# Kernel tuning notes

Measured on AMD Instinct MI355X. Metric: run time of the kernel, lower is better.

## Reference

```python
import jax, jax.numpy as jnp
import numpy as np

N = 100000      # nodes
E = 1600000     # edges (avg degree 16)
IN_DIM = 128
HID = 128
OUT = 10
EPS = 1e-5      # BatchNorm eps


def _lin(key, fan_in, fan_out):
    return jax.random.normal(key, (fan_in, fan_out), jnp.float32) * (1.0 / np.sqrt(fan_in))


def setup_inputs() -> dict:
    key = jax.random.key(0)
    ks = jax.random.split(key, 8)
    x = jax.random.normal(ks[0], (N, IN_DIM), jnp.float32)
    edge_index = jax.random.randint(ks[1], (2, E), 0, N, dtype=jnp.int64)
    return {
        "x": x,
        "edge_index": edge_index,
        "W0": _lin(ks[2], IN_DIM, HID), "b0": jnp.zeros((HID,), jnp.float32),
        "g0": jnp.ones((HID,), jnp.float32), "be0": jnp.zeros((HID,), jnp.float32),
        "W1": _lin(ks[3], HID, HID), "b1": jnp.zeros((HID,), jnp.float32),
        "g1": jnp.ones((HID,), jnp.float32), "be1": jnp.zeros((HID,), jnp.float32),
        "W2": _lin(ks[4], HID, OUT), "b2": jnp.zeros((OUT,), jnp.float32),
    }


def gcn_conv(x, W, b, src, dst, n):
    # PyG GCNConv: add self-loops, symmetric normalization D^-1/2 A D^-1/2.
    # deg includes the self-loop (+1).
    e = src.shape[0]
    deg = jax.ops.segment_sum(jnp.ones((e,), x.dtype), dst, num_segments=n) + 1.0
    dinv = jax.lax.rsqrt(deg)                     # deg >= 1 always
    norm = dinv[src] * dinv[dst]                  # [E]
    h = x @ W                                     # [N, out]
    msgs = h[src] * norm[:, None]                 # gather + scale, [E, out]
    agg = jax.ops.segment_sum(msgs, dst, num_segments=n)
    agg = agg + h * (dinv * dinv)[:, None]        # self-loop contribution
    return agg + b


def batch_norm(x, gamma, beta):
    mu = jnp.mean(x, axis=0)
    var = jnp.mean(jnp.square(x - mu), axis=0)    # biased var, as torch BN training
    return gamma * (x - mu) * jax.lax.rsqrt(var + EPS) + beta


def reference(x, edge_index, W0, b0, g0, be0, W1, b1, g1, be1, W2, b2):
    src, dst = edge_index[0], edge_index[1]
    h = jax.nn.relu(batch_norm(gcn_conv(x, W0, b0, src, dst, N), g0, be0))
    h = jax.nn.relu(batch_norm(gcn_conv(h, W1, b1, src, dst, N), g1, be1))
    return gcn_conv(h, W2, b2, src, dst, N)
```

## Files before the change

kernel.cpp:

```cpp
#include <hip/hip_runtime.h>
#include <hip/hip_bf16.h>

static constexpr int NN  = 100000;
static constexpr int NE  = 1600000;
static constexpr int DIM = 128;
static constexpr int OC  = 10;
static constexpr int BK  = 64;
static constexpr float BN_EPS = 1e-5f;
static constexpr float INVN   = 1.0f / (float)NN;

static constexpr int BINS = 391;
static constexpr int CAP  = 8176;
static constexpr int EPB  = 2048;
static constexpr int P1B  = (NE + EPB - 1) / EPB;

typedef unsigned short ushortT;
typedef unsigned int uintT;
typedef __attribute__((ext_vector_type(8))) short short8;
typedef __attribute__((ext_vector_type(4))) float floatx4;

__device__ __forceinline__ ushortT f2bf(float f) {
    union { float f; unsigned int i; } c;
    c.f = f;
    unsigned int r = c.i + 0x7FFFu + ((c.i >> 16) & 1u);
    return (ushortT)(r >> 16);
}

__device__ __forceinline__ uintT pack2(float lo, float hi) {
    return (uintT)f2bf(lo) | ((uintT)f2bf(hi) << 16);
}

__device__ __forceinline__ float4 f4fma(const float4 w, const float s, const float4 acc) {
    float4 r;
    r.x = fmaf(w.x, s, acc.x);
    r.y = fmaf(w.y, s, acc.y);
    r.z = fmaf(w.z, s, acc.z);
    r.w = fmaf(w.w, s, acc.w);
    return r;
}

__device__ __forceinline__ void acc8(const uint4 u, float* a) {
    a[0] += __uint_as_float(u.x << 16);
    a[1] += __uint_as_float(u.x & 0xFFFF0000u);
    a[2] += __uint_as_float(u.y << 16);
    a[3] += __uint_as_float(u.y & 0xFFFF0000u);
    a[4] += __uint_as_float(u.z << 16);
    a[5] += __uint_as_float(u.z & 0xFFFF0000u);
    a[6] += __uint_as_float(u.w << 16);
    a[7] += __uint_as_float(u.w & 0xFFFF0000u);
}

__device__ __forceinline__ void fma8(const uint4 u, float s, float* a) {
    a[0] = fmaf(__uint_as_float(u.x << 16),          s, a[0]);
    a[1] = fmaf(__uint_as_float(u.x & 0xFFFF0000u),  s, a[1]);
    a[2] = fmaf(__uint_as_float(u.y << 16),          s, a[2]);
    a[3] = fmaf(__uint_as_float(u.y & 0xFFFF0000u),  s, a[3]);
    a[4] = fmaf(__uint_as_float(u.z << 16),          s, a[4]);
    a[5] = fmaf(__uint_as_float(u.z & 0xFFFF0000u),  s, a[5]);
    a[6] = fmaf(__uint_as_float(u.w << 16),          s, a[6]);
    a[7] = fmaf(__uint_as_float(u.w & 0xFFFF0000u),  s, a[7]);
}

__device__ __forceinline__ void unp8(const uint4 u, float* a) {
    a[0] = __uint_as_float(u.x << 16);
    a[1] = __uint_as_float(u.x & 0xFFFF0000u);
    a[2] = __uint_as_float(u.y << 16);
    a[3] = __uint_as_float(u.y & 0xFFFF0000u);
    a[4] = __uint_as_float(u.z << 16);
    a[5] = __uint_as_float(u.z & 0xFFFF0000u);
    a[6] = __uint_as_float(u.w << 16);
    a[7] = __uint_as_float(u.w & 0xFFFF0000u);
}

__global__ void k_wt(const float* __restrict__ W0, const float* __restrict__ W1,
                     ushortT* __restrict__ WT0, ushortT* __restrict__ WT1,
                     float* __restrict__ stats) {
    int i = blockIdx.x * 256 + threadIdx.x;
    if (i < 1024) stats[i] = 0.f;
    int half = i >> 14, r = i & 16383;
    int n = r >> 7, k = r & 127;
    if (half == 0) WT0[r] = f2bf(W0[k * 128 + n]);
    else           WT1[r] = f2bf(W1[k * 128 + n]);
}

struct P1S {
    uint2 stage[EPB];
    int lcnt[BINS];
    int lbase[512];
    int lcur[BINS];
    int goff[BINS];
};
union SMu {
    P1S p1;
    ushortT xs[32 * 136];
};

__global__ __launch_bounds__(256)
void k_p1(const int* __restrict__ src, const int* __restrict__ dst,
          uint2* __restrict__ gbin, int* __restrict__ gcur,
          const float* __restrict__ x, const ushortT* __restrict__ WT,
          ushortT* __restrict__ outb)
{
    __shared__ SMu sm;
    const int idx = blockIdx.x;
    const int tid = threadIdx.x;
    const int d5 = idx / 5;
    if (idx - 5 * d5 == 0) {
        P1S& S = sm.p1;
        const int e00 = d5 * EPB;
        for (int b = tid; b < BINS; b += 256) S.lcnt[b] = 0;
        __syncthreads();
        int4 dv[2], sv[2];
        bool val[2];
        #pragma unroll
        for (int i = 0; i < 2; ++i) {
            int e0 = e00 + i * 1024 + tid * 4;
            val[i] = (e0 < NE);
            if (val[i]) {
                dv[i] = *(const int4*)(dst + e0);
                sv[i] = *(const int4*)(src + e0);
                atomicAdd(&S.lcnt[dv[i].x >> 8], 1);
                atomicAdd(&S.lcnt[dv[i].y >> 8], 1);
                atomicAdd(&S.lcnt[dv[i].z >> 8], 1);
                atomicAdd(&S.lcnt[dv[i].w >> 8], 1);
            }
        }
        __syncthreads();
        for (int b = tid; b < 512; b += 256) S.lbase[b] = (b < BINS) ? S.lcnt[b] : 0;
        __syncthreads();
        for (int off = 1; off < 512; off <<= 1) {
            int v0 = (tid >= off) ? S.lbase[tid - off] : 0;
            int c0 = S.lbase[tid];
            int v1 = S.lbase[tid + 256 - off];
            int c1 = S.lbase[tid + 256];
            __syncthreads();
            S.lbase[tid] = c0 + v0;
            S.lbase[tid + 256] = c1 + v1;
            __syncthreads();
        }
        for (int b = tid; b < BINS; b += 256) S.lcur[b] = b ? S.lbase[b - 1] : 0;
        __syncthreads();
        #pragma unroll
        for (int i = 0; i < 2; ++i) {
            if (val[i]) {
                int p;
                p = atomicAdd(&S.lcur[dv[i].x >> 8], 1);
                S.stage[p] = make_uint2((uintT)dv[i].x, (uintT)sv[i].x);
                p = atomicAdd(&S.lcur[dv[i].y >> 8], 1);
                S.stage[p] = make_uint2((uintT)dv[i].y, (uintT)sv[i].y);
                p = atomicAdd(&S.lcur[dv[i].z >> 8], 1);
                S.stage[p] = make_uint2((uintT)dv[i].z, (uintT)sv[i].z);
                p = atomicAdd(&S.lcur[dv[i].w >> 8], 1);
                S.stage[p] = make_uint2((uintT)dv[i].w, (uintT)sv[i].w);
            }
        }
        __syncthreads();
        for (int b = tid; b < BINS; b += 256) {
            int c = S.lcnt[b];
            int r = (c + 7) & ~7;
            S.goff[b] = r ? atomicAdd(&gcur[b], r) : 0;
        }
        __syncthreads();
        const int total = S.lbase[BINS - 1];
        for (int p = tid; p < total; p += 256) {
            uint2 e = S.stage[p];
            int bin = (int)(e.x >> 8);
            int eb = bin ? S.lbase[bin - 1] : 0;
            int gpos = S.goff[bin] + (p - eb);
            if (gpos < CAP) gbin[(size_t)bin * CAP + gpos] = e;
        }
        for (int b = tid; b < BINS; b += 256) {
            int c = S.lcnt[b];
            int r = (c + 7) & ~7;
            for (int q = c; q < r; ++q) {
                int gpos = S.goff[b] + q;
                if (gpos < CAP) gbin[(size_t)b * CAP + gpos] = make_uint2(0xFFFFFFFFu, 0u);
            }
        }
        return;
    }
    const int m = idx - d5 - 1;
    ushortT* XS = sm.xs;
    const int row0 = m * 32;

    #pragma unroll
    for (int i = 0; i < 4; ++i) {
        int id2 = tid + 256 * i;
        int rr = id2 >> 5, c4 = id2 & 31;
        int grow = row0 + rr;
        float4 v = {0.f, 0.f, 0.f, 0.f};
        if (grow < NN) v = ((const float4*)(x + (size_t)grow * DIM))[c4];
        ushort4 o;
        o.x = f2bf(v.x); o.y = f2bf(v.y); o.z = f2bf(v.z); o.w = f2bf(v.w);
        *(ushort4*)(XS + rr * 136 + c4 * 4) = o;
    }
    __syncthreads();

    const int w    = tid >> 6;
    const int lane = tid & 63;
    const int q    = lane >> 4;
    const int mr   = lane & 15;
    const int rw   = (w >> 1) * 16;
    const int ch   = (w & 1) * 64;

    floatx4 acc[4];
    #pragma unroll
    for (int t = 0; t < 4; ++t) { acc[t][0] = 0.f; acc[t][1] = 0.f; acc[t][2] = 0.f; acc[t][3] = 0.f; }

    #pragma unroll
    for (int c = 0; c < 4; ++c) {
        short8 a = *(const short8*)(XS + (rw + mr) * 136 + c * 32 + q * 8);
        #pragma unroll
        for (int t = 0; t < 4; ++t) {
            short8 b = *(const short8*)(WT + (size_t)(ch + t * 16 + mr) * 128 + c * 32 + q * 8);
            acc[t] = __builtin_amdgcn_mfma_f32_16x16x32_bf16(a, b, acc[t], 0, 0, 0);
        }
    }

    #pragma unroll
    for (int rr = 0; rr < 4; ++rr) {
        int grow = row0 + rw + q * 4 + rr;
        if (grow < NN) {
            #pragma unroll
            for (int t = 0; t < 4; ++t)
                outb[(size_t)grow * DIM + ch + t * 16 + mr] = f2bf(acc[t][rr]);
        }
    }
}

__global__ __launch_bounds__(512)
void k_p2(const uint2* __restrict__ gbin, const int* __restrict__ gcur,
          int* __restrict__ bucket, int* __restrict__ cnt,
          float* __restrict__ dinv)
{
    __shared__ int lc[256];
    const int b = blockIdx.x;
    const int tid = threadIdx.x;
    if (tid < 256) lc[tid] = 0;
    __syncthreads();
    int cb = gcur[b];
    if (cb > CAP) cb = CAP;
    const uint2* gb = gbin + (size_t)b * CAP;
    for (int p = tid; p < cb; p += 512) {
        uint2 e = gb[p];
        if (e.x != 0xFFFFFFFFu) {
            int slot = atomicAdd(&lc[e.x & 255], 1);
            if (slot < BK) bucket[(size_t)e.x * BK + slot] = (int)e.y;
        }
    }
    __syncthreads();
    if (tid < 256) {
        int n = b * 256 + tid;
        if (n < NN) {
            int d = lc[tid];
            cnt[n] = d;
            dinv[n] = rsqrtf((float)d + 1.0f);
        }
    }
}

template <bool EDGE_SCALE>
__global__ __launch_bounds__(256)
void k_agg_wide(const ushortT* __restrict__ hb, const int* __restrict__ cnt,
                const int* __restrict__ bucket, const float* __restrict__ dinv,
                const float* __restrict__ bias, ushortT* __restrict__ outBb,
                float* __restrict__ stats)
{
    const int lane = threadIdx.x & 63;
    const int w    = threadIdx.x >> 6;
    const int sg   = lane >> 4;
    const int f    = lane & 15;
    const int wid  = blockIdx.x * 4 + w;
    const int nW   = gridDim.x * 4;
    const uint4* h4 = (const uint4*)hb;

    float bl[8];
    #pragma unroll
    for (int i = 0; i < 8; ++i) bl[i] = bias[f * 8 + i];

    float ssum[8], ssq[8];
    #pragma unroll
    for (int i = 0; i < 8; ++i) { ssum[i] = 0.f; ssq[i] = 0.f; }

    for (int n = wid; n < NN; n += nW) {
        int d = cnt[n];
        if (d > BK) d = BK;
        const int* bp = bucket + (size_t)n * BK;
        float a[8];
        #pragma unroll
        for (int i = 0; i < 8; ++i) a[i] = 0.f;

        int j = 0;
        for (; j + 16 <= d; j += 16) {
            int4 pv = *(const int4*)(bp + j + 4 * sg);
            uint4 u0 = h4[(size_t)pv.x * 16 + f];
            uint4 u1 = h4[(size_t)pv.y * 16 + f];
            uint4 u2 = h4[(size_t)pv.z * 16 + f];
            uint4 u3 = h4[(size_t)pv.w * 16 + f];
            if (EDGE_SCALE) {
                float d0 = dinv[pv.x], d1 = dinv[pv.y];
                float d2 = dinv[pv.z], d3 = dinv[pv.w];
                fma8(u0, d0, a);
                fma8(u1, d1, a);
                fma8(u2, d2, a);
                fma8(u3, d3, a);
            } else {
                acc8(u0, a);
                acc8(u1, a);
                acc8(u2, a);
                acc8(u3, a);
            }
        }
        for (; j + 8 <= d; j += 8) {
            int s0 = bp[j + sg];
            int s1 = bp[j + 4 + sg];
            uint4 u0 = h4[(size_t)s0 * 16 + f];
            uint4 u1 = h4[(size_t)s1 * 16 + f];
            if (EDGE_SCALE) {
                float d0 = dinv[s0], d1 = dinv[s1];
                fma8(u0, d0, a);
                fma8(u1, d1, a);
            } else {
                acc8(u0, a);
                acc8(u1, a);
            }
        }
        for (; j < d; j += 4) {
            int e = j + sg;
            if (e < d) {
                int s0 = bp[e];
                uint4 u = h4[(size_t)s0 * 16 + f];
                if (EDGE_SCALE) fma8(u, dinv[s0], a);
                else            acc8(u, a);
            }
        }
        #pragma unroll
        for (int i = 0; i < 8; ++i) {
            a[i] += __shfl_xor(a[i], 16);
            a[i] += __shfl_xor(a[i], 32);
        }
        if (lane < 16) {
            uint4 us = h4[(size_t)n * 16 + f];
            float di = dinv[n];
            if (EDGE_SCALE) fma8(us, di, a);
            else            acc8(us, a);
            float v[8];
            #pragma unroll
            for (int i = 0; i < 8; ++i) v[i] = fmaf(di, a[i], bl[i]);
            uint4 o;
            o.x = pack2(v[0], v[1]);
            o.y = pack2(v[2], v[3]);
            o.z = pack2(v[4], v[5]);
            o.w = pack2(v[6], v[7]);
            ((uint4*)(outBb + (size_t)n * DIM))[f] = o;
            #pragma unroll
            for (int i = 0; i < 8; ++i) {
                ssum[i] += v[i];
                ssq[i]  = fmaf(v[i], v[i], ssq[i]);
            }
        }
    }

    __shared__ float ls[4 * 128], lq[4 * 128];
    if (lane < 16) {
        #pragma unroll
        for (int i = 0; i < 8; ++i) {
            ls[w * 128 + f * 8 + i] = ssum[i];
            lq[w * 128 + f * 8 + i] = ssq[i];
        }
    }
    __syncthreads();
    int t = threadIdx.x;
    if (t < 128) {
        float a = ls[t] + ls[128 + t] + ls[256 + t] + ls[384 + t];
        float b = lq[t] + lq[128 + t] + lq[256 + t] + lq[384 + t];
        unsafeAtomicAdd(&stats[t], a);
        unsafeAtomicAdd(&stats[128 + t], b);
    }
}

__global__ __launch_bounds__(256)
void k_mm128_l1(const ushortT* __restrict__ inb, const ushortT* __restrict__ WT,
                const float* __restrict__ stats, const float* __restrict__ g,
                const float* __restrict__ be, const float* __restrict__ dinv,
                ushortT* __restrict__ outb)
{
    __shared__ ushortT XS[64 * 136];
    __shared__ float CA[128], CD[128];
    const int tid  = threadIdx.x;
    const int row0 = blockIdx.x * 64;

    if (tid < 128) {
        float mu  = stats[tid] * INVN;
        float var = stats[128 + tid] * INVN - mu * mu;
        float a = g[tid] * rsqrtf(var + BN_EPS);
        CA[tid] = a;
        CD[tid] = be[tid] - mu * a;
    }
    __syncthreads();

    #pragma unroll
    for (int i = 0; i < 4; ++i) {
        int idx = tid + 256 * i;
        int r = idx >> 4, c8 = idx & 15;
        int grow = row0 + r;
        uint4 u = {0, 0, 0, 0};
        if (grow < NN) u = ((const uint4*)(inb + (size_t)grow * DIM))[c8];
        float v[8];
        unp8(u, v);
        #pragma unroll
        for (int k = 0; k < 8; ++k)
            v[k] = fmaxf(0.f, fmaf(v[k], CA[c8 * 8 + k], CD[c8 * 8 + k]));
        uint4 o;
        o.x = pack2(v[0], v[1]);
        o.y = pack2(v[2], v[3]);
        o.z = pack2(v[4], v[5]);
        o.w = pack2(v[6], v[7]);
        *(uint4*)(XS + r * 136 + c8 * 8) = o;
    }
    __syncthreads();

    const int w    = tid >> 6;
    const int lane = tid & 63;
    const int q    = lane >> 4;
    const int mr   = lane & 15;
    const int rw   = w * 16;

    floatx4 acc[8];
    #pragma unroll
    for (int t = 0; t < 8; ++t) { acc[t][0] = 0.f; acc[t][1] = 0.f; acc[t][2] = 0.f; acc[t][3] = 0.f; }

    #pragma unroll
    for (int c = 0; c < 4; ++c) {
        short8 a = *(const short8*)(XS + (rw + mr) * 136 + c * 32 + q * 8);
        #pragma unroll
        for (int t = 0; t < 8; ++t) {
            short8 b = *(const short8*)(WT + (size_t)(t * 16 + mr) * 128 + c * 32 + q * 8);
            acc[t] = __builtin_amdgcn_mfma_f32_16x16x32_bf16(a, b, acc[t], 0, 0, 0);
        }
    }

    #pragma unroll
    for (int r = 0; r < 4; ++r) {
        int grow = row0 + rw + q * 4 + r;
        if (grow < NN) {
            float di = dinv[grow];
            #pragma unroll
            for (int t = 0; t < 8; ++t) {
                outb[(size_t)grow * DIM + t * 16 + mr] = f2bf(acc[t][r] * di);
            }
        }
    }
}

__global__ __launch_bounds__(128)
void k_mm_l2(const ushortT* __restrict__ inb, const float* __restrict__ W2,
             const float* __restrict__ stats, const float* __restrict__ g,
             const float* __restrict__ be, const float* __restrict__ dinv,
             ushortT* __restrict__ Cb)
{
    __shared__ float WL[128 * 16];
    __shared__ float XS[32 * 128];
    __shared__ float CA[128], CD[128];
    const int tid  = threadIdx.x;
    const int row0 = blockIdx.x * 32;

    {
        float mu  = stats[tid] * INVN;
        float var = stats[128 + tid] * INVN - mu * mu;
        float a = g[tid] * rsqrtf(var + BN_EPS);
        CA[tid] = a;
        CD[tid] = be[tid] - mu * a;
    }
    for (int idx = tid; idx < 128 * 16; idx += 128) {
        int k = idx >> 4, c = idx & 15;
        WL[idx] = (c < OC) ? W2[k * OC + c] : 0.0f;
    }
    __syncthreads();

    #pragma unroll
    for (int i = 0; i < 4; ++i) {
        int idx = tid + 128 * i;
        int r = idx >> 4, c8 = idx & 15;
        uint4 u = ((const uint4*)(inb + (size_t)(row0 + r) * DIM))[c8];
        float v[8];
        unp8(u, v);
        float* xp = XS + r * 128 + c8 * 8;
        #pragma unroll
        for (int k = 0; k < 8; ++k)
            xp[k] = fmaxf(0.f, fmaf(v[k], CA[c8 * 8 + k], CD[c8 * 8 + k]));
    }
    __syncthreads();

    const int cg = tid & 3;
    const int rg = tid >> 2;
    float4 acc = {0, 0, 0, 0};
    const float4* XS4 = (const float4*)XS;
    const float4* WL4 = (const float4*)WL;
    for (int k = 0; k < 128; k += 4) {
        float4 w0 = WL4[(k + 0) * 4 + cg];
        float4 w1 = WL4[(k + 1) * 4 + cg];
        float4 w2 = WL4[(k + 2) * 4 + cg];
        float4 w3 = WL4[(k + 3) * 4 + cg];
        float4 x = XS4[rg * 32 + (k >> 2)];
        acc = f4fma(w0, x.x, f4fma(w1, x.y, f4fma(w2, x.z, f4fma(w3, x.w, acc))));
    }
    float di = dinv[row0 + rg];
    uint2 o;
    o.x = pack2(acc.x * di, acc.y * di);
    o.y = pack2(acc.z * di, acc.w * di);
    ((uint2*)(Cb + ((size_t)row0 + rg) * 16))[cg] = o;
}

__global__ __launch_bounds__(256)
void k_agg10(const ushortT* __restrict__ Cb, const int* __restrict__ cnt,
             const int* __restrict__ bucket, const float* __restrict__ dinv,
             const float* __restrict__ b2, float* __restrict__ out)
{
    const int lane = threadIdx.x & 63;
    const int sg   = lane >> 3;
    const int f    = lane & 7;
    const int wid  = (blockIdx.x * 256 + threadIdx.x) >> 6;
    const int nW   = gridDim.x * 4;
    const uintT* Cu = (const uintT*)Cb;

    for (int n = wid; n < NN; n += nW) {
        int d = cnt[n];
        if (d > BK) d = BK;
        const int* bp = bucket + (size_t)n * BK;
        float a0 = 0.f, a1 = 0.f;
        for (int j = sg; j < d; j += 8) {
            uintT u = Cu[(size_t)bp[j] * 8 + f];
            a0 += __uint_as_float(u << 16);
            a1 += __uint_as_float(u & 0xFFFF0000u);
        }
        a0 += __shfl_xor(a0, 8);  a1 += __shfl_xor(a1, 8);
        a0 += __shfl_xor(a0, 16); a1 += __shfl_xor(a1, 16);
        a0 += __shfl_xor(a0, 32); a1 += __shfl_xor(a1, 32);
        if (lane < 8) {
            uintT us = Cu[(size_t)n * 8 + f];
            a0 += __uint_as_float(us << 16);
            a1 += __uint_as_float(us & 0xFFFF0000u);
            float di = dinv[n];
            if (2 * f < OC) {
                float2 o;
                o.x = fmaf(di, a0, b2[2 * f]);
                o.y = fmaf(di, a1, b2[2 * f + 1]);
                *(float2*)(out + (size_t)n * OC + 2 * f) = o;
            }
        }
    }
}

extern "C" void kernel_launch(void* const* d_in, const int* in_sizes, int n_in,
                              void* d_out, int out_size, void* d_ws, size_t ws_size,
                              hipStream_t stream) {
    const float* x    = (const float*)d_in[0];
    const int*   ei   = (const int*)d_in[1];
    const int*   srcv = ei;
    const int*   dstv = ei + NE;
    const float* W0  = (const float*)d_in[2];
    const float* b0  = (const float*)d_in[3];
    const float* g0  = (const float*)d_in[4];
    const float* be0 = (const float*)d_in[5];
    const float* W1  = (const float*)d_in[6];
    const float* b1  = (const float*)d_in[7];
    const float* g1  = (const float*)d_in[8];
    const float* be1 = (const float*)d_in[9];
    const float* W2  = (const float*)d_in[10];
    const float* b2  = (const float*)d_in[11];
    float* out = (float*)d_out;

    float* base   = (float*)d_ws;
    int*   cnt    = (int*)base;
    float* dinv   = base + NN;
    float* stats  = base + 2 * NN;
    int*   gcur   = (int*)(stats + 512);
    ushortT* WT0  = (ushortT*)(base + 2 * NN + 1024);
    ushortT* WT1  = (ushortT*)(base + 2 * NN + 9216);
    int*   bucket = (int*)(base + 2 * NN + 17408);
    ushortT* A_bf = (ushortT*)(base + 2 * NN + 17408 + (size_t)NN * BK);
    ushortT* B_bf = A_bf + (size_t)NN * DIM;
    ushortT* Cb   = A_bf;
    uint2* gbin   = (uint2*)B_bf;

    k_wt<<<128, 256, 0, stream>>>(W0, W1, WT0, WT1, stats);

    k_p1<<<P1B + 3125, 256, 0, stream>>>(srcv, dstv, gbin, gcur, x, WT0, A_bf);
    k_p2<<<BINS, 512, 0, stream>>>(gbin, gcur, bucket, cnt, dinv);

    k_agg_wide<true><<<2048, 256, 0, stream>>>(A_bf, cnt, bucket, dinv, b0, B_bf, stats);

    k_mm128_l1<<<(NN + 63) / 64, 256, 0, stream>>>(B_bf, WT1, stats, g0, be0, dinv, A_bf);
    k_agg_wide<false><<<2048, 256, 0, stream>>>(A_bf, cnt, bucket, dinv, b1, B_bf, stats + 256);

    k_mm_l2<<<NN / 32, 128, 0, stream>>>(B_bf, W2, stats + 256, g1, be1, dinv, Cb);
    k_agg10<<<1024, 256, 0, stream>>>(Cb, cnt, bucket, dinv, b2, out);
}
```

Baseline: 493.4 us.

## Halve destination bins to 512 nodes each and use wave-shuffle scan

```diff
diff --git a/kernel.cpp b/kernel.cpp
--- a/kernel.cpp
+++ b/kernel.cpp
@@ -9,8 +9,8 @@
 static constexpr float BN_EPS = 1e-5f;
 static constexpr float INVN   = 1.0f / (float)NN;
 
-static constexpr int BINS = 391;
-static constexpr int CAP  = 8176;
+static constexpr int BINS = 196;
+static constexpr int CAP  = 16320;
 static constexpr int EPB  = 2048;
 static constexpr int P1B  = (NE + EPB - 1) / EPB;
 
@@ -86,9 +86,10 @@
 struct P1S {
     uint2 stage[EPB];
     int lcnt[BINS];
-    int lbase[512];
+    int lbase[256];
     int lcur[BINS];
     int goff[BINS];
+    int wsum[4];
 };
 union SMu {
     P1S p1;
@@ -108,7 +109,7 @@
     if (idx - 5 * d5 == 0) {
         P1S& S = sm.p1;
         const int e00 = d5 * EPB;
-        for (int b = tid; b < BINS; b += 256) S.lcnt[b] = 0;
+        if (tid < BINS) S.lcnt[tid] = 0;
         __syncthreads();
         int4 dv[2], sv[2];
         bool val[2];
@@ -119,62 +120,65 @@
             if (val[i]) {
                 dv[i] = *(const int4*)(dst + e0);
                 sv[i] = *(const int4*)(src + e0);
-                atomicAdd(&S.lcnt[dv[i].x >> 8], 1);
-                atomicAdd(&S.lcnt[dv[i].y >> 8], 1);
-                atomicAdd(&S.lcnt[dv[i].z >> 8], 1);
-                atomicAdd(&S.lcnt[dv[i].w >> 8], 1);
+                atomicAdd(&S.lcnt[dv[i].x >> 9], 1);
+                atomicAdd(&S.lcnt[dv[i].y >> 9], 1);
+                atomicAdd(&S.lcnt[dv[i].z >> 9], 1);
+                atomicAdd(&S.lcnt[dv[i].w >> 9], 1);
             }
         }
         __syncthreads();
-        for (int b = tid; b < 512; b += 256) S.lbase[b] = (b < BINS) ? S.lcnt[b] : 0;
+        int v = (tid < BINS) ? S.lcnt[tid] : 0;
+        #pragma unroll
+        for (int dd = 1; dd < 64; dd <<= 1) {
+            int t = __shfl_up(v, dd);
+            if ((tid & 63) >= dd) v += t;
+        }
+        if ((tid & 63) == 63) S.wsum[tid >> 6] = v;
         __syncthreads();
-        for (int off = 1; off < 512; off <<= 1) {
-            int v0 = (tid >= off) ? S.lbase[tid - off] : 0;
-            int c0 = S.lbase[tid];
-            int v1 = S.lbase[tid + 256 - off];
-            int c1 = S.lbase[tid + 256];
-            __syncthreads();
-            S.lbase[tid] = c0 + v0;
-            S.lbase[tid + 256] = c1 + v1;
-            __syncthreads();
-        }
-        for (int b = tid; b < BINS; b += 256) S.lcur[b] = b ? S.lbase[b - 1] : 0;
+        if (tid >= 64) {
+            int off = S.wsum[0];
+            if (tid >= 128) off += S.wsum[1];
+            if (tid >= 192) off += S.wsum[2];
+            v += off;
+        }
+        S.lbase[tid] = v;
+        if (tid < BINS) S.lcur[tid] = v - S.lcnt[tid];
         __syncthreads();
         #pragma unroll
         for (int i = 0; i < 2; ++i) {
             if (val[i]) {
                 int p;
-                p = atomicAdd(&S.lcur[dv[i].x >> 8], 1);
+                p = atomicAdd(&S.lcur[dv[i].x >> 9], 1);
                 S.stage[p] = make_uint2((uintT)dv[i].x, (uintT)sv[i].x);
-                p = atomicAdd(&S.lcur[dv[i].y >> 8], 1);
+                p = atomicAdd(&S.lcur[dv[i].y >> 9], 1);
                 S.stage[p] = make_uint2((uintT)dv[i].y, (uintT)sv[i].y);
-                p = atomicAdd(&S.lcur[dv[i].z >> 8], 1);
+                p = atomicAdd(&S.lcur[dv[i].z >> 9], 1);
                 S.stage[p] = make_uint2((uintT)dv[i].z, (uintT)sv[i].z);
-                p = atomicAdd(&S.lcur[dv[i].w >> 8], 1);
+                p = atomicAdd(&S.lcur[dv[i].w >> 9], 1);
                 S.stage[p] = make_uint2((uintT)dv[i].w, (uintT)sv[i].w);
             }
         }
         __syncthreads();
-        for (int b = tid; b < BINS; b += 256) {
-            int c = S.lcnt[b];
+        if (tid < BINS) {
+            int c = S.lcnt[tid];
             int r = (c + 7) & ~7;
-            S.goff[b] = r ? atomicAdd(&gcur[b], r) : 0;
+            S.goff[tid] = r ? atomicAdd(&gcur[tid], r) : 0;
         }
         __syncthreads();
         const int total = S.lbase[BINS - 1];
         for (int p = tid; p < total; p += 256) {
             uint2 e = S.stage[p];
-            int bin = (int)(e.x >> 8);
+            int bin = (int)(e.x >> 9);
             int eb = bin ? S.lbase[bin - 1] : 0;
             int gpos = S.goff[bin] + (p - eb);
             if (gpos < CAP) gbin[(size_t)bin * CAP + gpos] = e;
         }
-        for (int b = tid; b < BINS; b += 256) {
-            int c = S.lcnt[b];
+        if (tid < BINS) {
+            int c = S.lcnt[tid];
             int r = (c + 7) & ~7;
             for (int q = c; q < r; ++q) {
-                int gpos = S.goff[b] + q;
-                if (gpos < CAP) gbin[(size_t)b * CAP + gpos] = make_uint2(0xFFFFFFFFu, 0u);
+                int gpos = S.goff[tid] + q;
+                if (gpos < CAP) gbin[(size_t)tid * CAP + gpos] = make_uint2(0xFFFFFFFFu, 0u);
             }
         }
         return;
@@ -233,10 +237,10 @@
           int* __restrict__ bucket, int* __restrict__ cnt,
           float* __restrict__ dinv)
 {
-    __shared__ int lc[256];
+    __shared__ int lc[512];
     const int b = blockIdx.x;
     const int tid = threadIdx.x;
-    if (tid < 256) lc[tid] = 0;
+    lc[tid] = 0;
     __syncthreads();
     int cb = gcur[b];
     if (cb > CAP) cb = CAP;
@@ -244,13 +248,13 @@
     for (int p = tid; p < cb; p += 512) {
         uint2 e = gb[p];
         if (e.x != 0xFFFFFFFFu) {
-            int slot = atomicAdd(&lc[e.x & 255], 1);
+            int slot = atomicAdd(&lc[e.x & 511], 1);
             if (slot < BK) bucket[(size_t)e.x * BK + slot] = (int)e.y;
         }
     }
     __syncthreads();
-    if (tid < 256) {
-        int n = b * 256 + tid;
+    {
+        int n = b * 512 + tid;
         if (n < NN) {
             int d = lc[tid];
             cnt[n] = d;
```

Result: no change. 496.6 us (+0.7%).
